# Kernel optimization log

Hardware: AMD Instinct MI355X
Metric: run time of the kernel (lower is better)

The kernel has to match this reference:

```python
import jax, jax.numpy as jnp
import numpy as np
import math

B, N, E = 4, 20000, 320000
CIN, SD, CF, TF = 4, 2, 8, 4
W, L, S, H, FFN, OUT = 256, 4, 64, 8, 1024, 4
D = W // H
EPS = 1e-6  # graph_bias_eps


def _layer_norm(x, w, b):
    mu = jnp.mean(x, -1, keepdims=True)
    var = jnp.mean((x - mu) ** 2, -1, keepdims=True)
    return (x - mu) * jax.lax.rsqrt(var + 1e-5) * w + b


def _aggregate(row, col, vals, x):
    # sparse adj (N,N) @ x per batch: y[b,i] = sum_e vals[e] * x[b, col[e]] for row[e]==i
    def one(xb):
        return jax.ops.segment_sum(vals[:, None] * xb[col], row, num_segments=N)
    return jax.vmap(one)(x)


def setup_inputs() -> dict:
    key = jax.random.key(0)
    ks = jax.random.split(key, 24)
    def n(i, shape, scale=0.02):
        return jax.random.normal(ks[i], shape, dtype=jnp.float32) * scale
    inp = {}
    inp['fields'] = jax.random.normal(ks[0], (B, N, CIN), dtype=jnp.float32)
    inp['coords'] = jax.random.uniform(ks[1], (B, N, SD), dtype=jnp.float32)
    inp['t_norm'] = jax.random.uniform(ks[2], (B,), dtype=jnp.float32)
    inp['adj_values'] = jax.random.uniform(ks[3], (E,), dtype=jnp.float32)
    # --- parameters ---
    inp['freq_matrix'] = jax.random.normal(ks[4], (SD, CF), dtype=jnp.float32)
    inp['omega'] = 1000.0 ** (-jnp.arange(TF, dtype=jnp.float32) / TF)
    inp['in_w'] = n(5, (CIN + 2 * CF + 2 * TF, W)); inp['in_b'] = jnp.zeros((W,), jnp.float32)
    inp['ln1_w'] = jnp.ones((L, W), jnp.float32); inp['ln1_b'] = jnp.zeros((L, W), jnp.float32)
    inp['ln2_w'] = jnp.ones((L, W), jnp.float32); inp['ln2_b'] = jnp.zeros((L, W), jnp.float32)
    inp['slice_w'] = n(6, (L, W, S)); inp['slice_b'] = jnp.zeros((L, S), jnp.float32)
    inp['q_w'] = n(7, (L, W, W)); inp['q_b'] = jnp.zeros((L, W), jnp.float32)
    inp['k_w'] = n(8, (L, W, W)); inp['k_b'] = jnp.zeros((L, W), jnp.float32)
    inp['v_w'] = n(9, (L, W, W)); inp['v_b'] = jnp.zeros((L, W), jnp.float32)
    inp['o_w'] = n(10, (L, W, W)); inp['o_b'] = jnp.zeros((L, W), jnp.float32)
    inp['beta_raw'] = jnp.full((L,), math.log(math.expm1(0.13)), jnp.float32)
    inp['ffn1_w'] = n(11, (L, W, FFN)); inp['ffn1_b'] = jnp.zeros((L, FFN), jnp.float32)
    inp['ffn2_w'] = n(12, (L, FFN, W)); inp['ffn2_b'] = jnp.zeros((L, W), jnp.float32)
    inp['out_w'] = n(13, (W, OUT)); inp['out_b'] = jnp.zeros((OUT,), jnp.float32)
    inp['adj_indices'] = jax.random.randint(ks[14], (2, E), 0, N, dtype=jnp.int32)
    return inp


def reference(fields, coords, t_norm, adj_values, freq_matrix, omega, in_w, in_b,
              ln1_w, ln1_b, ln2_w, ln2_b, slice_w, slice_b, q_w, q_b, k_w, k_b,
              v_w, v_b, o_w, o_b, beta_raw, ffn1_w, ffn1_b, ffn2_w, ffn2_b,
              out_w, out_b, adj_indices):
    row, col = adj_indices[0], adj_indices[1]
    # spatial + temporal encoders
    sp = 2.0 * jnp.pi * (coords @ freq_matrix)
    spat = jnp.concatenate([jnp.sin(sp), jnp.cos(sp)], -1)               # (B,N,2*CF)
    ang = (t_norm * 1000.0)[:, None] * omega[None, :]
    temb = jnp.concatenate([jnp.sin(ang), jnp.cos(ang)], -1)             # (B,2*TF)
    temb = jnp.broadcast_to(temb[:, None, :], (B, N, 2 * TF))
    h = jnp.concatenate([fields, spat, temb], -1) @ in_w + in_b          # (B,N,W)
    for l in range(L):
        # ---- GraphBiasAttention on norm1(h) ----
        hn = _layer_norm(h, ln1_w[l], ln1_b[l])
        weights = jax.nn.softmax(hn @ slice_w[l] + slice_b[l], -1)       # (B,N,S)
        wsum = jnp.maximum(weights.sum(1), EPS)                          # (B,S)
        slices = jnp.einsum('bns,bnc->bsc', weights, hn) / wsum[..., None]
        gw = _aggregate(row, col, adj_values, weights)                   # (B,N,S)
        gb = jnp.einsum('bns,bnt->bst', weights, gw)                     # (B,S,S)
        gb = 0.5 * (gb + gb.transpose(0, 2, 1))
        gb = gb / jnp.maximum(gb.sum(-1, keepdims=True), EPS)
        gb = jnp.log(jnp.maximum(gb, EPS))
        q = (slices @ q_w[l] + q_b[l]).reshape(B, S, H, D).transpose(0, 2, 1, 3)
        k = (slices @ k_w[l] + k_b[l]).reshape(B, S, H, D).transpose(0, 2, 1, 3)
        v = (slices @ v_w[l] + v_b[l]).reshape(B, S, H, D).transpose(0, 2, 1, 3)
        logits = jnp.einsum('bhsd,bhtd->bhst', q, k) / math.sqrt(D)
        logits = logits + jax.nn.softplus(beta_raw[l]) * gb[:, None]
        attn = jax.nn.softmax(logits, -1)
        so = jnp.einsum('bhst,bhtd->bhsd', attn, v).transpose(0, 2, 1, 3).reshape(B, S, W)
        so = so @ o_w[l] + o_b[l]
        h = h + jnp.einsum('bns,bsc->bnc', weights, so)
        # ---- FFN ----
        hn2 = _layer_norm(h, ln2_w[l], ln2_b[l])
        h = h + (jax.nn.gelu(hn2 @ ffn1_w[l] + ffn1_b[l], approximate=False) @ ffn2_w[l] + ffn2_b[l])
    return h @ out_w + out_b                                             # (B,N,OUT)
```

## Files before the change

### kernel.cpp

```cpp
#include <hip/hip_runtime.h>
#include <math.h>

#define BB 4
#define NN 20000
#define NE 320000
#define WW 256
#define SS 64
#define NH 8
#define HD 32
#define NF 1024
#define NL 4
#define GEPS 1e-6f

typedef __attribute__((ext_vector_type(8))) short short8v;
typedef __attribute__((ext_vector_type(4))) float f32x4;

static __device__ __forceinline__ short f2bf(float x){
  union { float f; unsigned u; } v; v.f = x;
  unsigned r = v.u + 0x7fffu + ((v.u >> 16) & 1u);
  return (short)(r >> 16);
}
static __device__ __forceinline__ float bfu_lo(unsigned u){
  union { unsigned u; float f; } v; v.u = u << 16; return v.f;
}
static __device__ __forceinline__ float bfu_hi(unsigned u){
  union { unsigned u; float f; } v; v.u = u & 0xffff0000u; return v.f;
}
static __device__ __forceinline__ float gelu_f(float x){
  return 0.5f*x*(1.0f + erff(x*0.70710678118654752f));
}

#define GLOAD16(gsrc, ldst) \
  __builtin_amdgcn_global_load_lds( \
      (const __attribute__((address_space(1))) void*)(gsrc), \
      (__attribute__((address_space(3))) void*)(ldst), 16, 0, 0)

__global__ __launch_bounds__(256) void k_embed(
    const float* __restrict__ fields, const float* __restrict__ coords,
    const float* __restrict__ t_norm, const float* __restrict__ freq,
    const float* __restrict__ omega, const float* __restrict__ in_w,
    const float* __restrict__ in_b, float* __restrict__ h)
{
  __shared__ float inv[16][28];
  __shared__ float temb[8];
  const int t = threadIdx.x;
  const size_t tok0 = (size_t)blockIdx.x * 16;
  const int b = (int)(tok0 / NN);
  if (t < 8) {
    int f = t & 3;
    float ang = t_norm[b] * 1000.0f * omega[f];
    temb[t] = (t < 4) ? sinf(ang) : cosf(ang);
  }
  if (t < 128) {
    int tok = t >> 3, f = t & 7;
    size_t n = tok0 + tok;
    float c0 = coords[n*2+0], c1 = coords[n*2+1];
    float sp = 6.283185307179586f * (c0*freq[f] + c1*freq[8+f]);
    inv[tok][4+f]  = sinf(sp);
    inv[tok][12+f] = cosf(sp);
  } else if (t < 192) {
    int idx = t - 128; int tok = idx >> 2, i = idx & 3;
    inv[tok][i] = fields[(tok0+tok)*4 + i];
  }
  __syncthreads();
  if (t < 128) {
    int tok = t >> 3, f = t & 7;
    inv[tok][20+f] = temb[f];
  }
  __syncthreads();
  float acc[16];
  float bias = in_b[t];
  #pragma unroll
  for (int i = 0; i < 16; i++) acc[i] = bias;
  #pragma unroll 4
  for (int k = 0; k < 28; k++) {
    float w = in_w[k*WW + t];
    #pragma unroll
    for (int i = 0; i < 16; i++) acc[i] += inv[i][k]*w;
  }
  #pragma unroll
  for (int i = 0; i < 16; i++) h[(tok0+i)*WW + t] = acc[i];
}

__global__ __launch_bounds__(256) void k_lnw(
    const float* __restrict__ h, const float* __restrict__ lnw,
    const float* __restrict__ lnb, const float* __restrict__ sw,
    const float* __restrict__ sb, float* __restrict__ wts,
    short* __restrict__ wtsb, float* __restrict__ mu_rstd)
{
  __shared__ float hn[16][WW];
  __shared__ float ps[16][16], pq[16][16];
  __shared__ float mus[16], rss[16];
  const int t = threadIdx.x;
  const size_t tok0 = (size_t)blockIdx.x * 16;
  const int tok = t >> 4, seg = t & 15;
  {
    const float4* hp = (const float4*)(h + (tok0+tok)*WW + seg*16);
    float sum = 0.f, sq = 0.f;
    #pragma unroll
    for (int i = 0; i < 4; i++){
      float4 v = hp[i];
      sum += v.x+v.y+v.z+v.w;
      sq  += v.x*v.x+v.y*v.y+v.z*v.z+v.w*v.w;
      *((float4*)&hn[tok][seg*16 + i*4]) = v;
    }
    ps[tok][seg] = sum; pq[tok][seg] = sq;
  }
  __syncthreads();
  if (t < 16){
    float s0=0.f, q0=0.f;
    #pragma unroll
    for (int i = 0; i < 16; i++){ s0 += ps[t][i]; q0 += pq[t][i]; }
    float mu = s0*(1.0f/WW);
    float var = q0*(1.0f/WW) - mu*mu;
    float rs = rsqrtf(var + 1e-5f);
    mus[t] = mu; rss[t] = rs;
    mu_rstd[(tok0 + t)*2]     = mu;
    mu_rstd[(tok0 + t)*2 + 1] = rs;
  }
  __syncthreads();
  {
    float mu = mus[tok], rs = rss[tok];
    #pragma unroll
    for (int i = 0; i < 16; i++){
      int c = seg*16 + i;
      hn[tok][c] = (hn[tok][c]-mu)*rs*lnw[c] + lnb[c];
    }
  }
  __syncthreads();
  const int s = t & 63, tg = t >> 6;
  float acc[4];
  float bs = sb[s];
  #pragma unroll
  for (int i = 0; i < 4; i++) acc[i] = bs;
  for (int c4 = 0; c4 < 64; c4++){
    float w0 = sw[(c4*4+0)*SS + s];
    float w1 = sw[(c4*4+1)*SS + s];
    float w2 = sw[(c4*4+2)*SS + s];
    float w3 = sw[(c4*4+3)*SS + s];
    #pragma unroll
    for (int i = 0; i < 4; i++){
      float4 hv = *((const float4*)&hn[tg*4+i][c4*4]);
      acc[i] += hv.x*w0 + hv.y*w1 + hv.z*w2 + hv.w*w3;
    }
  }
  #pragma unroll
  for (int i = 0; i < 4; i++){
    float m = acc[i];
    #pragma unroll
    for (int off = 32; off > 0; off >>= 1) m = fmaxf(m, __shfl_xor(m, off));
    float e = expf(acc[i] - m);
    float ssum = e;
    #pragma unroll
    for (int off = 32; off > 0; off >>= 1) ssum += __shfl_xor(ssum, off);
    float wv = e/ssum;
    wts[(tok0 + tg*4 + i)*SS + s] = wv;
    wtsb[(tok0 + tg*4 + i)*SS + s] = f2bf(wv);
  }
}

__global__ __launch_bounds__(256) void k_slices(
    const float* __restrict__ h, const float* __restrict__ wts,
    const float* __restrict__ mu_rstd, const float* __restrict__ lnw,
    const float* __restrict__ lnb, float* __restrict__ sacc,
    float* __restrict__ wsum)
{
  __shared__ float wstage[16][SS];
  const int t = threadIdx.x;
  const int b = blockIdx.y;
  const int n0 = blockIdx.x * 128;
  const float lw = lnw[t], lb = lnb[t];
  float acc[SS];
  #pragma unroll
  for (int s = 0; s < SS; s++) acc[s] = 0.f;
  float wsl = 0.f;
  for (int it = 0; it < 8; it++){
    int nb = n0 + it*16;
    {
      int tk = t >> 4, s4 = (t & 15)*4;
      int n = nb + tk;
      float4 v = make_float4(0.f,0.f,0.f,0.f);
      if (n < NN) v = *((const float4*)(wts + ((size_t)b*NN + n)*SS + s4));
      *((float4*)&wstage[tk][s4]) = v;
    }
    __syncthreads();
    #pragma unroll 4
    for (int tk = 0; tk < 16; tk++){
      int n = nb + tk;
      if (n < NN){
        size_t g = (size_t)b*NN + n;
        float mu = mu_rstd[g*2], rsd = mu_rstd[g*2+1];
        float hv = h[g*WW + t];
        float hnv = (hv-mu)*rsd*lw + lb;
        #pragma unroll
        for (int s4 = 0; s4 < 16; s4++){
          float4 wv = *((const float4*)&wstage[tk][s4*4]);
          acc[s4*4+0] += wv.x*hnv;
          acc[s4*4+1] += wv.y*hnv;
          acc[s4*4+2] += wv.z*hnv;
          acc[s4*4+3] += wv.w*hnv;
        }
      }
    }
    if (t < SS){
      #pragma unroll
      for (int tk = 0; tk < 16; tk++) wsl += wstage[tk][t];
    }
    __syncthreads();
  }
  #pragma unroll
  for (int s = 0; s < SS; s++)
    atomicAdd(&sacc[((size_t)b*SS + s)*WW + t], acc[s]);
  if (t < SS) atomicAdd(&wsum[b*SS + t], wsl);
}

__global__ __launch_bounds__(256) void k_slices_fin(
    const float* __restrict__ sacc, const float* __restrict__ wsum,
    float* __restrict__ slices)
{
  int i = blockIdx.x*256 + threadIdx.x;
  int sidx = i >> 8;
  float ws = fmaxf(wsum[sidx], GEPS);
  slices[i] = sacc[i] / ws;
}

#define GB_BLKS 1000
#define GB_PB   250
#define GB_EDG  (NE/GB_PB)
__global__ __launch_bounds__(256) void k_gb2(
    const short* __restrict__ wtsb, const int* __restrict__ adj,
    const float* __restrict__ vals, float* __restrict__ gb)
{
  __shared__ float gbw[SS*SS];
  const int t = threadIdx.x;
  const int bid = blockIdx.x;
  const int xcd = bid & 7;
  const int b = xcd >> 1;
  const int grp = (bid >> 3)*2 + (xcd & 1);
  const int e0 = grp * GB_EDG;
  const int w = t >> 6, l = t & 63;
  const int sg = l >> 3, tg = l & 7;
  #pragma unroll
  for (int i = 0; i < 16; i++) gbw[t + 256*i] = 0.f;
  __syncthreads();
  float acc[8][8];
  #pragma unroll
  for (int i = 0; i < 8; i++)
    #pragma unroll
    for (int u = 0; u < 8; u++) acc[i][u] = 0.f;
  const short* wb = wtsb + (size_t)b*NN*SS;
  for (int e = e0 + w; e < e0 + GB_EDG; e += 8){
    int row0 = adj[e],     col0 = adj[NE + e];
    int row1 = adj[e + 4], col1 = adj[NE + e + 4];
    float v0 = vals[e], v1 = vals[e + 4];
    uint4 ru0 = *(const uint4*)(wb + (size_t)row0*SS + sg*8);
    uint4 cu0 = *(const uint4*)(wb + (size_t)col0*SS + tg*8);
    uint4 ru1 = *(const uint4*)(wb + (size_t)row1*SS + sg*8);
    uint4 cu1 = *(const uint4*)(wb + (size_t)col1*SS + tg*8);
    float rr[8], cc[8];
    rr[0]=bfu_lo(ru0.x)*v0; rr[1]=bfu_hi(ru0.x)*v0;
    rr[2]=bfu_lo(ru0.y)*v0; rr[3]=bfu_hi(ru0.y)*v0;
    rr[4]=bfu_lo(ru0.z)*v0; rr[5]=bfu_hi(ru0.z)*v0;
    rr[6]=bfu_lo(ru0.w)*v0; rr[7]=bfu_hi(ru0.w)*v0;
    cc[0]=bfu_lo(cu0.x); cc[1]=bfu_hi(cu0.x);
    cc[2]=bfu_lo(cu0.y); cc[3]=bfu_hi(cu0.y);
    cc[4]=bfu_lo(cu0.z); cc[5]=bfu_hi(cu0.z);
    cc[6]=bfu_lo(cu0.w); cc[7]=bfu_hi(cu0.w);
    #pragma unroll
    for (int i = 0; i < 8; i++)
      #pragma unroll
      for (int u = 0; u < 8; u++) acc[i][u] += rr[i]*cc[u];
    rr[0]=bfu_lo(ru1.x)*v1; rr[1]=bfu_hi(ru1.x)*v1;
    rr[2]=bfu_lo(ru1.y)*v1; rr[3]=bfu_hi(ru1.y)*v1;
    rr[4]=bfu_lo(ru1.z)*v1; rr[5]=bfu_hi(ru1.z)*v1;
    rr[6]=bfu_lo(ru1.w)*v1; rr[7]=bfu_hi(ru1.w)*v1;
    cc[0]=bfu_lo(cu1.x); cc[1]=bfu_hi(cu1.x);
    cc[2]=bfu_lo(cu1.y); cc[3]=bfu_hi(cu1.y);
    cc[4]=bfu_lo(cu1.z); cc[5]=bfu_hi(cu1.z);
    cc[6]=bfu_lo(cu1.w); cc[7]=bfu_hi(cu1.w);
    #pragma unroll
    for (int i = 0; i < 8; i++)
      #pragma unroll
      for (int u = 0; u < 8; u++) acc[i][u] += rr[i]*cc[u];
  }
  #pragma unroll
  for (int i = 0; i < 8; i++)
    #pragma unroll
    for (int u = 0; u < 8; u++)
      atomicAdd(&gbw[(sg*8+i)*SS + tg*8 + u], acc[i][u]);
  __syncthreads();
  #pragma unroll
  for (int i = 0; i < 16; i++){
    int idx = t + 256*i;
    atomicAdd(&gb[(size_t)b*SS*SS + idx], gbw[idx]);
  }
}

__global__ __launch_bounds__(256) void k_gbfin(
    const float* __restrict__ gbin, float* __restrict__ gbout,
    const float* __restrict__ beta_raw, int layer)
{
  __shared__ float g[SS*SS];
  __shared__ float gs[SS*SS];
  __shared__ float rs[SS];
  const int t = threadIdx.x;
  const int b = blockIdx.x;
  #pragma unroll
  for (int i = 0; i < 16; i++) g[t + 256*i] = gbin[(size_t)b*SS*SS + t + 256*i];
  __syncthreads();
  #pragma unroll
  for (int i = 0; i < 16; i++){
    int idx = t + 256*i; int r = idx >> 6, c = idx & 63;
    gs[idx] = 0.5f*(g[idx] + g[c*SS + r]);
  }
  __syncthreads();
  if (t < SS){
    float sum = 0.f;
    for (int c = 0; c < SS; c++) sum += gs[t*SS + c];
    rs[t] = 1.0f / fmaxf(sum, GEPS);
  }
  __syncthreads();
  float beta = log1pf(expf(beta_raw[layer]));
  #pragma unroll
  for (int i = 0; i < 16; i++){
    int idx = t + 256*i; int r = idx >> 6;
    gbout[(size_t)b*SS*SS + idx] = beta * logf(fmaxf(gs[idx]*rs[r], GEPS));
  }
}

__global__ __launch_bounds__(256) void k_attn(
    const float* __restrict__ slices,
    const float* __restrict__ qw, const float* __restrict__ qb,
    const float* __restrict__ kw, const float* __restrict__ kb,
    const float* __restrict__ vw, const float* __restrict__ vb,
    const float* __restrict__ gbf, float* __restrict__ so)
{
  __shared__ float sl[SS][WW];
  __shared__ float qh[SS][HD], kh[SS][HD], vh[SS][HD];
  __shared__ float att[SS][SS];
  const int t = threadIdx.x;
  const int hh = blockIdx.x, b = blockIdx.y;
  {
    const float4* sp4 = (const float4*)(slices + (size_t)b*SS*WW);
    float4* sl4 = (float4*)sl;
    #pragma unroll
    for (int i = 0; i < 16; i++) sl4[t + 256*i] = sp4[t + 256*i];
  }
  __syncthreads();
  const int s = t >> 2, dq = t & 3, d0 = dq*8;
  float aq[8], ak[8], av[8];
  #pragma unroll
  for (int j = 0; j < 8; j++){
    aq[j] = qb[hh*HD + d0 + j];
    ak[j] = kb[hh*HD + d0 + j];
    av[j] = vb[hh*HD + d0 + j];
  }
  for (int c = 0; c < WW; c++){
    float sv = sl[s][c];
    const float4* q4 = (const float4*)(qw + (size_t)c*WW + hh*HD + d0);
    const float4* k4 = (const float4*)(kw + (size_t)c*WW + hh*HD + d0);
    const float4* v4 = (const float4*)(vw + (size_t)c*WW + hh*HD + d0);
    float4 qa = q4[0], qc = q4[1];
    float4 ka = k4[0], kc = k4[1];
    float4 va = v4[0], vc = v4[1];
    aq[0]+=sv*qa.x; aq[1]+=sv*qa.y; aq[2]+=sv*qa.z; aq[3]+=sv*qa.w;
    aq[4]+=sv*qc.x; aq[5]+=sv*qc.y; aq[6]+=sv*qc.z; aq[7]+=sv*qc.w;
    ak[0]+=sv*ka.x; ak[1]+=sv*ka.y; ak[2]+=sv*ka.z; ak[3]+=sv*ka.w;
    ak[4]+=sv*kc.x; ak[5]+=sv*kc.y; ak[6]+=sv*kc.z; ak[7]+=sv*kc.w;
    av[0]+=sv*va.x; av[1]+=sv*va.y; av[2]+=sv*va.z; av[3]+=sv*va.w;
    av[4]+=sv*vc.x; av[5]+=sv*vc.y; av[6]+=sv*vc.z; av[7]+=sv*vc.w;
  }
  *((float4*)&qh[s][d0])   = make_float4(aq[0],aq[1],aq[2],aq[3]);
  *((float4*)&qh[s][d0+4]) = make_float4(aq[4],aq[5],aq[6],aq[7]);
  *((float4*)&kh[s][d0])   = make_float4(ak[0],ak[1],ak[2],ak[3]);
  *((float4*)&kh[s][d0+4]) = make_float4(ak[4],ak[5],ak[6],ak[7]);
  *((float4*)&vh[s][d0])   = make_float4(av[0],av[1],av[2],av[3]);
  *((float4*)&vh[s][d0+4]) = make_float4(av[4],av[5],av[6],av[7]);
  __syncthreads();
  float qreg[HD];
  #pragma unroll
  for (int d4 = 0; d4 < 8; d4++){
    float4 qv = *((const float4*)&qh[s][d4*4]);
    qreg[d4*4+0]=qv.x; qreg[d4*4+1]=qv.y; qreg[d4*4+2]=qv.z; qreg[d4*4+3]=qv.w;
  }
  const int tc0 = dq*16;
  float lg[16];
  #pragma unroll
  for (int u = 0; u < 16; u++){
    float a = 0.f;
    #pragma unroll
    for (int d4 = 0; d4 < 8; d4++){
      float4 kv = *((const float4*)&kh[tc0+u][d4*4]);
      a += qreg[d4*4+0]*kv.x + qreg[d4*4+1]*kv.y + qreg[d4*4+2]*kv.z + qreg[d4*4+3]*kv.w;
    }
    lg[u] = a*0.17677669529663687f + gbf[((size_t)b*SS + s)*SS + tc0 + u];
  }
  float m = lg[0];
  #pragma unroll
  for (int u = 1; u < 16; u++) m = fmaxf(m, lg[u]);
  m = fmaxf(m, __shfl_xor(m, 1));
  m = fmaxf(m, __shfl_xor(m, 2));
  float ssum = 0.f;
  #pragma unroll
  for (int u = 0; u < 16; u++){ lg[u] = expf(lg[u]-m); ssum += lg[u]; }
  ssum += __shfl_xor(ssum, 1);
  ssum += __shfl_xor(ssum, 2);
  float invs = 1.0f/ssum;
  #pragma unroll
  for (int u = 0; u < 16; u++) att[s][tc0+u] = lg[u]*invs;
  __syncthreads();
  float ao[8];
  #pragma unroll
  for (int j = 0; j < 8; j++) ao[j] = 0.f;
  for (int t2 = 0; t2 < SS; t2++){
    float a = att[s][t2];
    float4 v0 = *((const float4*)&vh[t2][d0]);
    float4 v1 = *((const float4*)&vh[t2][d0+4]);
    ao[0]+=a*v0.x; ao[1]+=a*v0.y; ao[2]+=a*v0.z; ao[3]+=a*v0.w;
    ao[4]+=a*v1.x; ao[5]+=a*v1.y; ao[6]+=a*v1.z; ao[7]+=a*v1.w;
  }
  float* sop = so + ((size_t)b*SS + s)*WW + hh*HD + d0;
  *((float4*)sop)     = make_float4(ao[0],ao[1],ao[2],ao[3]);
  *((float4*)(sop+4)) = make_float4(ao[4],ao[5],ao[6],ao[7]);
}

__global__ __launch_bounds__(256) void k_oproj(
    const float* __restrict__ so, const float* __restrict__ ow,
    const float* __restrict__ ob, float* __restrict__ so_out)
{
  __shared__ float st[16][WW];
  const int t = threadIdx.x;
  const int b = blockIdx.y;
  const int s0 = blockIdx.x * 16;
  {
    const float4* sp = (const float4*)(so + ((size_t)b*SS + s0)*WW);
    float4* st4 = (float4*)st;
    #pragma unroll
    for (int i = 0; i < 4; i++) st4[t + 256*i] = sp[t + 256*i];
  }
  __syncthreads();
  float acc[16];
  float bias = ob[t];
  #pragma unroll
  for (int i = 0; i < 16; i++) acc[i] = bias;
  for (int k4 = 0; k4 < 64; k4++){
    float w0 = ow[(size_t)(k4*4+0)*WW + t];
    float w1 = ow[(size_t)(k4*4+1)*WW + t];
    float w2 = ow[(size_t)(k4*4+2)*WW + t];
    float w3 = ow[(size_t)(k4*4+3)*WW + t];
    #pragma unroll
    for (int i = 0; i < 16; i++){
      float4 sv = *((const float4*)&st[i][k4*4]);
      acc[i] += sv.x*w0 + sv.y*w1 + sv.z*w2 + sv.w*w3;
    }
  }
  #pragma unroll
  for (int i = 0; i < 16; i++)
    so_out[((size_t)b*SS + s0 + i)*WW + t] = acc[i];
}

__global__ __launch_bounds__(256) void k_hupd(
    const float* __restrict__ wts, const float* __restrict__ so_out,
    float* __restrict__ h)
{
  __shared__ float wst[64*SS];
  const int t = threadIdx.x;
  const int b = blockIdx.y;
  const int n0 = blockIdx.x * 128;
  float sc[SS];
  #pragma unroll
  for (int s = 0; s < SS; s++) sc[s] = so_out[((size_t)b*SS + s)*WW + t];
  for (int it = 0; it < 2; it++){
    int nb = n0 + it*64;
    {
      const float4* wsrc = (const float4*)(wts + ((size_t)b*NN + nb)*SS);
      #pragma unroll
      for (int i = 0; i < 4; i++){
        int jj = t + 256*i;
        int tk = jj >> 4;
        float4 v = make_float4(0.f,0.f,0.f,0.f);
        if (nb + tk < NN) v = wsrc[jj];
        *((float4*)&wst[jj*4]) = v;
      }
    }
    __syncthreads();
    for (int tk = 0; tk < 64; tk++){
      int n = nb + tk;
      if (n >= NN) break;
      float a = 0.f;
      #pragma unroll
      for (int s4 = 0; s4 < 16; s4++){
        float4 wv = *((const float4*)&wst[tk*SS + s4*4]);
        a += wv.x*sc[s4*4+0] + wv.y*sc[s4*4+1] + wv.z*sc[s4*4+2] + wv.w*sc[s4*4+3];
      }
      h[((size_t)b*NN + n)*WW + t] += a;
    }
    __syncthreads();
  }
}

__global__ __launch_bounds__(256) void k_tr1(
    const float* __restrict__ in, short* __restrict__ out)
{
  __shared__ float tile[32][33];
  const int tx = threadIdx.x & 31;
  const int ty = threadIdx.x >> 5;
  const size_t moff = (size_t)blockIdx.z * WW * NF;
  const int x = blockIdx.x*32 + tx;
  const int y0 = blockIdx.y*32;
  #pragma unroll
  for (int i = 0; i < 4; i++){
    int r = y0 + ty + i*8;
    tile[ty + i*8][tx] = in[moff + (size_t)r*NF + x];
  }
  __syncthreads();
  const int k = y0 + tx;
  #pragma unroll
  for (int i = 0; i < 4; i++){
    int j = blockIdx.x*32 + ty + i*8;
    int off = j*WW + ((((k>>3) ^ (j&7)))<<3) + (k&7);
    out[moff + off] = f2bf(tile[tx][ty + i*8]);
  }
}

__global__ __launch_bounds__(256) void k_tr2(
    const float* __restrict__ in, short* __restrict__ out)
{
  __shared__ float tile[32][33];
  const int tx = threadIdx.x & 31;
  const int ty = threadIdx.x >> 5;
  const size_t moff = (size_t)blockIdx.z * NF * WW;
  const int x = blockIdx.x*32 + tx;
  const int y0 = blockIdx.y*32;
  #pragma unroll
  for (int i = 0; i < 4; i++){
    int r = y0 + ty + i*8;
    tile[ty + i*8][tx] = in[moff + (size_t)r*WW + x];
  }
  __syncthreads();
  const int ch = y0 >> 5;
  const int jl = tx;
  #pragma unroll
  for (int i = 0; i < 4; i++){
    int c = blockIdx.x*32 + ty + i*8;
    int off = ch*8192 + c*32 + ((((jl>>3) ^ (c&3)))<<3) + (jl&7);
    out[moff + off] = f2bf(tile[tx][ty + i*8]);
  }
}

#define FTM 64
#define CH 32
__global__ __launch_bounds__(256, 4) void k_ffn7(
    float* __restrict__ h,
    const float* __restrict__ lnw, const float* __restrict__ lnb,
    const short* __restrict__ w1t, const float* __restrict__ b1,
    const short* __restrict__ w2t, const float* __restrict__ b2)
{
  __align__(16) __shared__ short w1s[CH*256];
  __align__(16) __shared__ short w2s[256*CH];
  __align__(16) __shared__ short gbuf[4][16*40];
  const int t = threadIdx.x;
  const int w = t >> 6, l = t & 63;
  const int lm = l & 15, g = l >> 4;
  const size_t tok0 = (size_t)blockIdx.x * FTM;
  const size_t tokA = tok0 + (size_t)w*16 + lm;
  short8v hn[8];
  {
    const float* hp = h + tokA*WW + g*8;
    float4 hv[16];
    float sum = 0.f, sq = 0.f;
    #pragma unroll
    for (int u = 0; u < 16; u++){
      float4 v = *(const float4*)(hp + (u>>1)*32 + (u&1)*4);
      hv[u] = v;
      sum += v.x+v.y+v.z+v.w;
      sq  += v.x*v.x+v.y*v.y+v.z*v.z+v.w*v.w;
    }
    sum += __shfl_xor(sum, 16); sum += __shfl_xor(sum, 32);
    sq  += __shfl_xor(sq, 16);  sq  += __shfl_xor(sq, 32);
    float mu = sum*(1.0f/WW);
    float var = sq*(1.0f/WW) - mu*mu;
    float rs = rsqrtf(var + 1e-5f);
    #pragma unroll
    for (int f = 0; f < 8; f++){
      float4 w0 = *(const float4*)(lnw + f*32 + g*8);
      float4 w1 = *(const float4*)(lnw + f*32 + g*8 + 4);
      float4 b0 = *(const float4*)(lnb + f*32 + g*8);
      float4 b1v = *(const float4*)(lnb + f*32 + g*8 + 4);
      float4 a = hv[f*2], bqv = hv[f*2+1];
      short8v fr;
      fr[0] = f2bf((a.x  -mu)*rs*w0.x + b0.x);
      fr[1] = f2bf((a.y  -mu)*rs*w0.y + b0.y);
      fr[2] = f2bf((a.z  -mu)*rs*w0.z + b0.z);
      fr[3] = f2bf((a.w  -mu)*rs*w0.w + b0.w);
      fr[4] = f2bf((bqv.x-mu)*rs*w1.x + b1v.x);
      fr[5] = f2bf((bqv.y-mu)*rs*w1.y + b1v.y);
      fr[6] = f2bf((bqv.z-mu)*rs*w1.z + b1v.z);
      fr[7] = f2bf((bqv.w-mu)*rs*w1.w + b1v.w);
      hn[f] = fr;
    }
  }
  f32x4 acc2[16];
  #pragma unroll
  for (int ct = 0; ct < 16; ct++)
    acc2[ct] = (f32x4){0.f,0.f,0.f,0.f};

  for (int ch = 0; ch < NF/CH; ch++){
    const int j0 = ch*CH;
    const short* w1c = w1t + (size_t)j0*256;
    const short* w2c = w2t + (size_t)ch*8192;
    #pragma unroll
    for (int it = 0; it < 4; it++){
      int p = w*4 + it;
      GLOAD16(w1c + p*512 + l*8, w1s + p*512);
      GLOAD16(w2c + p*512 + l*8, w2s + p*512);
    }
    __syncthreads();
    #pragma unroll
    for (int jt = 0; jt < 2; jt++){
      f32x4 d0 = (f32x4){0.f,0.f,0.f,0.f};
      const int rl = jt*16 + lm;
      #pragma unroll
      for (int ks = 0; ks < 8; ks++){
        short8v af = *(const short8v*)(w1s + rl*256 + ((((ks<<2)|g) ^ (rl&7))<<3));
        d0 = __builtin_amdgcn_mfma_f32_16x16x32_bf16(af, hn[ks], d0, 0, 0, 0);
      }
      float4 bb = *(const float4*)(b1 + j0 + jt*16 + g*4);
      float x0 = gelu_f(d0[0] + bb.x), x1 = gelu_f(d0[1] + bb.y);
      float x2 = gelu_f(d0[2] + bb.z), x3 = gelu_f(d0[3] + bb.w);
      unsigned u0 = (unsigned)(unsigned short)f2bf(x0) | ((unsigned)(unsigned short)f2bf(x1) << 16);
      unsigned u1 = (unsigned)(unsigned short)f2bf(x2) | ((unsigned)(unsigned short)f2bf(x3) << 16);
      *(uint2*)(&gbuf[w][lm*40 + jt*16 + g*4]) = make_uint2(u0, u1);
    }
    short8v gA0 = *(const short8v*)(&gbuf[w][lm*40 + g*8]);
    #pragma unroll
    for (int ct = 0; ct < 16; ct++){
      const int row = ct*16 + lm;
      short8v a0 = *(const short8v*)(w2s + row*32 + (((g ^ (row&3)))<<3));
      acc2[ct] = __builtin_amdgcn_mfma_f32_16x16x32_bf16(a0, gA0, acc2[ct], 0, 0, 0);
    }
    __syncthreads();
  }
  float* tb = (float*)&gbuf[w][0];
  const int tok_l = l >> 2, cq = (l & 3)*4;
  {
    const size_t trow = tok0 + (size_t)w*16;
    #pragma unroll
    for (int ct = 0; ct < 16; ct++){
      float4 sv;
      sv.x = acc2[ct][0]; sv.y = acc2[ct][1];
      sv.z = acc2[ct][2]; sv.w = acc2[ct][3];
      *(float4*)(&tb[lm*20 + g*4]) = sv;
      float4 tv = *(const float4*)(&tb[tok_l*20 + cq]);
      float4 bb = *(const float4*)(b2 + ct*16 + cq);
      float* hp = h + (trow + tok_l)*WW + ct*16 + cq;
      float4 ho = *(const float4*)hp;
      ho.x += tv.x + bb.x; ho.y += tv.y + bb.y;
      ho.z += tv.z + bb.z; ho.w += tv.w + bb.w;
      *(float4*)hp = ho;
    }
  }
}

__global__ __launch_bounds__(256) void k_out(
    const float* __restrict__ h, const float* __restrict__ ow,
    const float* __restrict__ ob, float* __restrict__ out)
{
  size_t n = (size_t)blockIdx.x*256 + threadIdx.x;
  if (n >= (size_t)BB*NN) return;
  float a0=ob[0], a1=ob[1], a2=ob[2], a3=ob[3];
  const float4* hp = (const float4*)(h + n*WW);
  const float4* ow4 = (const float4*)ow;
  for (int c4 = 0; c4 < 64; c4++){
    float4 hv = hp[c4];
    float4 w0 = ow4[c4*4+0], w1 = ow4[c4*4+1], w2 = ow4[c4*4+2], w3 = ow4[c4*4+3];
    a0 += hv.x*w0.x + hv.y*w1.x + hv.z*w2.x + hv.w*w3.x;
    a1 += hv.x*w0.y + hv.y*w1.y + hv.z*w2.y + hv.w*w3.y;
    a2 += hv.x*w0.z + hv.y*w1.z + hv.z*w2.z + hv.w*w3.z;
    a3 += hv.x*w0.w + hv.y*w1.w + hv.z*w2.w + hv.w*w3.w;
  }
  *((float4*)(out + n*4)) = make_float4(a0,a1,a2,a3);
}

extern "C" void kernel_launch(void* const* d_in, const int* in_sizes, int n_in,
                              void* d_out, int out_size, void* d_ws, size_t ws_size,
                              hipStream_t stream) {
  const float* fields    = (const float*)d_in[0];
  const float* coords    = (const float*)d_in[1];
  const float* t_norm    = (const float*)d_in[2];
  const float* adj_vals  = (const float*)d_in[3];
  const float* freq      = (const float*)d_in[4];
  const float* omega     = (const float*)d_in[5];
  const float* in_w      = (const float*)d_in[6];
  const float* in_b      = (const float*)d_in[7];
  const float* ln1_w     = (const float*)d_in[8];
  const float* ln1_b     = (const float*)d_in[9];
  const float* ln2_w     = (const float*)d_in[10];
  const float* ln2_b     = (const float*)d_in[11];
  const float* slice_w   = (const float*)d_in[12];
  const float* slice_b   = (const float*)d_in[13];
  const float* q_w       = (const float*)d_in[14];
  const float* q_b       = (const float*)d_in[15];
  const float* k_w       = (const float*)d_in[16];
  const float* k_b       = (const float*)d_in[17];
  const float* v_w       = (const float*)d_in[18];
  const float* v_b       = (const float*)d_in[19];
  const float* o_w       = (const float*)d_in[20];
  const float* o_b       = (const float*)d_in[21];
  const float* beta_raw  = (const float*)d_in[22];
  const float* ffn1_w    = (const float*)d_in[23];
  const float* ffn1_b    = (const float*)d_in[24];
  const float* ffn2_w    = (const float*)d_in[25];
  const float* ffn2_b    = (const float*)d_in[26];
  const float* out_w     = (const float*)d_in[27];
  const float* out_b     = (const float*)d_in[28];
  const int*   adj       = (const int*)d_in[29];
  float* out = (float*)d_out;

  float* ws = (float*)d_ws;
  size_t off = 0;
  float* h        = ws + off; off += (size_t)BB*NN*WW;
  float* wts      = ws + off; off += (size_t)BB*NN*SS;
  float* mu_rstd  = ws + off; off += (size_t)BB*NN*2;
  float* sacc     = ws + off; off += (size_t)BB*SS*WW;
  float* wsumb    = ws + off; off += (size_t)BB*SS;
  float* gb       = ws + off; off += (size_t)BB*SS*SS;
  float* gbf      = ws + off; off += (size_t)BB*SS*SS;
  float* slices   = ws + off; off += (size_t)BB*SS*WW;
  float* so       = ws + off; off += (size_t)BB*SS*WW;
  float* so_out   = ws + off; off += (size_t)BB*SS*WW;
  short* w1tb     = (short*)(ws + off); off += (size_t)NL*WW*NF/2;
  short* w2tb     = (short*)(ws + off); off += (size_t)NL*WW*NF/2;
  short* wtsb     = (short*)(ws + off); off += (size_t)BB*NN*SS/2;

  hipLaunchKernelGGL(k_tr1, dim3(NF/32, WW/32, NL), dim3(256), 0, stream,
      ffn1_w, w1tb);
  hipLaunchKernelGGL(k_tr2, dim3(WW/32, NF/32, NL), dim3(256), 0, stream,
      ffn2_w, w2tb);

  hipLaunchKernelGGL(k_embed, dim3(BB*NN/16), dim3(256), 0, stream,
      fields, coords, t_norm, freq, omega, in_w, in_b, h);

  for (int l = 0; l < NL; l++){
    hipMemsetAsync(sacc, 0,
        (size_t)(BB*SS*WW + BB*SS + BB*SS*SS)*sizeof(float), stream);
    hipLaunchKernelGGL(k_lnw, dim3(BB*NN/16), dim3(256), 0, stream,
        h, ln1_w + l*WW, ln1_b + l*WW,
        slice_w + (size_t)l*WW*SS, slice_b + l*SS, wts, wtsb, mu_rstd);
    hipLaunchKernelGGL(k_slices, dim3(157, BB), dim3(256), 0, stream,
        h, wts, mu_rstd, ln1_w + l*WW, ln1_b + l*WW, sacc, wsumb);
    hipLaunchKernelGGL(k_slices_fin, dim3(BB*SS*WW/256), dim3(256), 0, stream,
        sacc, wsumb, slices);
    hipLaunchKernelGGL(k_gb2, dim3(GB_BLKS), dim3(256), 0, stream,
        wtsb, adj, adj_vals, gb);
    hipLaunchKernelGGL(k_gbfin, dim3(BB), dim3(256), 0, stream,
        gb, gbf, beta_raw, l);
    hipLaunchKernelGGL(k_attn, dim3(NH, BB), dim3(256), 0, stream,
        slices,
        q_w + (size_t)l*WW*WW, q_b + l*WW,
        k_w + (size_t)l*WW*WW, k_b + l*WW,
        v_w + (size_t)l*WW*WW, v_b + l*WW,
        gbf, so);
    hipLaunchKernelGGL(k_oproj, dim3(4, BB), dim3(256), 0, stream,
        so, o_w + (size_t)l*WW*WW, o_b + l*WW, so_out);
    hipLaunchKernelGGL(k_hupd, dim3(157, BB), dim3(256), 0, stream,
        wts, so_out, h);
    hipLaunchKernelGGL(k_ffn7, dim3(BB*NN/FTM), dim3(256), 0, stream,
        h, ln2_w + l*WW, ln2_b + l*WW,
        w1tb + (size_t)l*WW*NF, ffn1_b + l*NF,
        w2tb + (size_t)l*WW*NF, ffn2_b + l*WW);
  }

  hipLaunchKernelGGL(k_out, dim3((BB*NN + 255)/256), dim3(256), 0, stream,
      h, out_w, out_b, out);
}
```

Measured before the change: 3.684 ms.

## Fuse slice-attention residual update into FFN kernel

Removes the separate k_hupd kernel and performs the weights@so_out residual update at the start of the FFN kernel. so_out is staged in shared memory in two halves, and the updated h feeds the layernorm statistics directly. This saves one full read-modify-write pass over h and one launch per layer. In exchange the grid becomes 2D per batch with a validity guard, and each token does its S=64 update with FP32 FMAs, which adds register pressure under the 4-blocks-per-CU launch bound.

```diff
diff --git a/kernel.cpp b/kernel.cpp
--- a/kernel.cpp
+++ b/kernel.cpp
@@ -459,46 +459,6 @@
     so_out[((size_t)b*SS + s0 + i)*WW + t] = acc[i];
 }
 
-__global__ __launch_bounds__(256) void k_hupd(
-    const float* __restrict__ wts, const float* __restrict__ so_out,
-    float* __restrict__ h)
-{
-  __shared__ float wst[64*SS];
-  const int t = threadIdx.x;
-  const int b = blockIdx.y;
-  const int n0 = blockIdx.x * 128;
-  float sc[SS];
-  #pragma unroll
-  for (int s = 0; s < SS; s++) sc[s] = so_out[((size_t)b*SS + s)*WW + t];
-  for (int it = 0; it < 2; it++){
-    int nb = n0 + it*64;
-    {
-      const float4* wsrc = (const float4*)(wts + ((size_t)b*NN + nb)*SS);
-      #pragma unroll
-      for (int i = 0; i < 4; i++){
-        int jj = t + 256*i;
-        int tk = jj >> 4;
-        float4 v = make_float4(0.f,0.f,0.f,0.f);
-        if (nb + tk < NN) v = wsrc[jj];
-        *((float4*)&wst[jj*4]) = v;
-      }
-    }
-    __syncthreads();
-    for (int tk = 0; tk < 64; tk++){
-      int n = nb + tk;
-      if (n >= NN) break;
-      float a = 0.f;
-      #pragma unroll
-      for (int s4 = 0; s4 < 16; s4++){
-        float4 wv = *((const float4*)&wst[tk*SS + s4*4]);
-        a += wv.x*sc[s4*4+0] + wv.y*sc[s4*4+1] + wv.z*sc[s4*4+2] + wv.w*sc[s4*4+3];
-      }
-      h[((size_t)b*NN + n)*WW + t] += a;
-    }
-    __syncthreads();
-  }
-}
-
 __global__ __launch_bounds__(256) void k_tr1(
     const float* __restrict__ in, short* __restrict__ out)
 {
@@ -550,60 +510,103 @@
 
 #define FTM 64
 #define CH 32
-__global__ __launch_bounds__(256, 4) void k_ffn7(
-    float* __restrict__ h,
+__global__ __launch_bounds__(256, 4) void k_ffn8(
+    float* __restrict__ h, const float* __restrict__ wts,
+    const float* __restrict__ so_out,
     const float* __restrict__ lnw, const float* __restrict__ lnb,
     const short* __restrict__ w1t, const float* __restrict__ b1,
     const short* __restrict__ w2t, const float* __restrict__ b2)
 {
-  __align__(16) __shared__ short w1s[CH*256];
-  __align__(16) __shared__ short w2s[256*CH];
+  __shared__ __align__(16) char wbig[32768];
   __align__(16) __shared__ short gbuf[4][16*40];
+  short* w1s = (short*)wbig;
+  short* w2s = (short*)(wbig + 16384);
+  float* sob = (float*)wbig;
   const int t = threadIdx.x;
   const int w = t >> 6, l = t & 63;
   const int lm = l & 15, g = l >> 4;
-  const size_t tok0 = (size_t)blockIdx.x * FTM;
-  const size_t tokA = tok0 + (size_t)w*16 + lm;
+  const int b = blockIdx.y;
+  const int ltok0 = blockIdx.x * FTM;
+  const bool valid = (ltok0 + w*16) < NN;
+  const int lA = valid ? (ltok0 + w*16 + lm) : lm;
+  const size_t tokA = (size_t)b*NN + lA;
+  float* hrow = h + tokA*WW;
+  const float* wrow = wts + tokA*SS;
+
+  float sum = 0.f, sq = 0.f;
+  #pragma unroll
+  for (int half = 0; half < 2; half++){
+    __syncthreads();
+    #pragma unroll
+    for (int it = 0; it < 8; it++){
+      int idx = it*256 + t;
+      int s = idx >> 5, c4 = (idx & 31) << 2;
+      GLOAD16(so_out + ((size_t)b*SS + s)*WW + half*128 + c4,
+              ((float*)sob) + (size_t)idx*4);
+    }
+    __syncthreads();
+    float4 hv[8], upd[8];
+    #pragma unroll
+    for (int u = 0; u < 8; u++){
+      hv[u] = *(const float4*)(hrow + (half*4 + (u>>1))*32 + g*8 + (u&1)*4);
+      upd[u] = make_float4(0.f,0.f,0.f,0.f);
+    }
+    #pragma unroll 2
+    for (int s4 = 0; s4 < 16; s4++){
+      float4 wv4 = *(const float4*)(wrow + s4*4);
+      #pragma unroll
+      for (int k = 0; k < 4; k++){
+        float wv = (k==0)?wv4.x:(k==1)?wv4.y:(k==2)?wv4.z:wv4.w;
+        const float* sor = sob + (s4*4+k)*128 + g*8;
+        #pragma unroll
+        for (int u = 0; u < 8; u++){
+          float4 so4 = *(const float4*)(sor + (u>>1)*32 + (u&1)*4);
+          upd[u].x += wv*so4.x; upd[u].y += wv*so4.y;
+          upd[u].z += wv*so4.z; upd[u].w += wv*so4.w;
+        }
+      }
+    }
+    #pragma unroll
+    for (int u = 0; u < 8; u++){
+      float4 nv;
+      nv.x = hv[u].x + upd[u].x; nv.y = hv[u].y + upd[u].y;
+      nv.z = hv[u].z + upd[u].z; nv.w = hv[u].w + upd[u].w;
+      sum += nv.x+nv.y+nv.z+nv.w;
+      sq  += nv.x*nv.x+nv.y*nv.y+nv.z*nv.z+nv.w*nv.w;
+      if (valid)
+        *(float4*)(hrow + (half*4 + (u>>1))*32 + g*8 + (u&1)*4) = nv;
+    }
+  }
+  sum += __shfl_xor(sum, 16); sum += __shfl_xor(sum, 32);
+  sq  += __shfl_xor(sq, 16);  sq  += __shfl_xor(sq, 32);
+  float mu = sum*(1.0f/WW);
+  float var = sq*(1.0f/WW) - mu*mu;
+  float rs = rsqrtf(var + 1e-5f);
   short8v hn[8];
-  {
-    const float* hp = h + tokA*WW + g*8;
-    float4 hv[16];
-    float sum = 0.f, sq = 0.f;
-    #pragma unroll
-    for (int u = 0; u < 16; u++){
-      float4 v = *(const float4*)(hp + (u>>1)*32 + (u&1)*4);
-      hv[u] = v;
-      sum += v.x+v.y+v.z+v.w;
-      sq  += v.x*v.x+v.y*v.y+v.z*v.z+v.w*v.w;
-    }
-    sum += __shfl_xor(sum, 16); sum += __shfl_xor(sum, 32);
-    sq  += __shfl_xor(sq, 16);  sq  += __shfl_xor(sq, 32);
-    float mu = sum*(1.0f/WW);
-    float var = sq*(1.0f/WW) - mu*mu;
-    float rs = rsqrtf(var + 1e-5f);
-    #pragma unroll
-    for (int f = 0; f < 8; f++){
-      float4 w0 = *(const float4*)(lnw + f*32 + g*8);
-      float4 w1 = *(const float4*)(lnw + f*32 + g*8 + 4);
-      float4 b0 = *(const float4*)(lnb + f*32 + g*8);
-      float4 b1v = *(const float4*)(lnb + f*32 + g*8 + 4);
-      float4 a = hv[f*2], bqv = hv[f*2+1];
-      short8v fr;
-      fr[0] = f2bf((a.x  -mu)*rs*w0.x + b0.x);
-      fr[1] = f2bf((a.y  -mu)*rs*w0.y + b0.y);
-      fr[2] = f2bf((a.z  -mu)*rs*w0.z + b0.z);
-      fr[3] = f2bf((a.w  -mu)*rs*w0.w + b0.w);
-      fr[4] = f2bf((bqv.x-mu)*rs*w1.x + b1v.x);
-      fr[5] = f2bf((bqv.y-mu)*rs*w1.y + b1v.y);
-      fr[6] = f2bf((bqv.z-mu)*rs*w1.z + b1v.z);
-      fr[7] = f2bf((bqv.w-mu)*rs*w1.w + b1v.w);
-      hn[f] = fr;
-    }
+  #pragma unroll
+  for (int f = 0; f < 8; f++){
+    float4 a  = *(const float4*)(hrow + f*32 + g*8);
+    float4 bq = *(const float4*)(hrow + f*32 + g*8 + 4);
+    float4 w0 = *(const float4*)(lnw + f*32 + g*8);
+    float4 w1 = *(const float4*)(lnw + f*32 + g*8 + 4);
+    float4 b0 = *(const float4*)(lnb + f*32 + g*8);
+    float4 b1v = *(const float4*)(lnb + f*32 + g*8 + 4);
+    short8v fr;
+    fr[0] = f2bf((a.x -mu)*rs*w0.x + b0.x);
+    fr[1] = f2bf((a.y -mu)*rs*w0.y + b0.y);
+    fr[2] = f2bf((a.z -mu)*rs*w0.z + b0.z);
+    fr[3] = f2bf((a.w -mu)*rs*w0.w + b0.w);
+    fr[4] = f2bf((bq.x-mu)*rs*w1.x + b1v.x);
+    fr[5] = f2bf((bq.y-mu)*rs*w1.y + b1v.y);
+    fr[6] = f2bf((bq.z-mu)*rs*w1.z + b1v.z);
+    fr[7] = f2bf((bq.w-mu)*rs*w1.w + b1v.w);
+    hn[f] = fr;
   }
   f32x4 acc2[16];
   #pragma unroll
   for (int ct = 0; ct < 16; ct++)
     acc2[ct] = (f32x4){0.f,0.f,0.f,0.f};
+  __syncthreads();
 
   for (int ch = 0; ch < NF/CH; ch++){
     const int j0 = ch*CH;
@@ -641,10 +644,10 @@
     }
     __syncthreads();
   }
-  float* tb = (float*)&gbuf[w][0];
-  const int tok_l = l >> 2, cq = (l & 3)*4;
-  {
-    const size_t trow = tok0 + (size_t)w*16;
+  if (valid){
+    float* tb = (float*)&gbuf[w][0];
+    const int tok_l = l >> 2, cq = (l & 3)*4;
+    const size_t trow = (size_t)b*NN + ltok0 + w*16;
     #pragma unroll
     for (int ct = 0; ct < 16; ct++){
       float4 sv;
@@ -763,10 +766,8 @@
         gbf, so);
     hipLaunchKernelGGL(k_oproj, dim3(4, BB), dim3(256), 0, stream,
         so, o_w + (size_t)l*WW*WW, o_b + l*WW, so_out);
-    hipLaunchKernelGGL(k_hupd, dim3(157, BB), dim3(256), 0, stream,
-        wts, so_out, h);
-    hipLaunchKernelGGL(k_ffn7, dim3(BB*NN/FTM), dim3(256), 0, stream,
-        h, ln2_w + l*WW, ln2_b + l*WW,
+    hipLaunchKernelGGL(k_ffn8, dim3((NN + FTM - 1)/FTM, BB), dim3(256), 0, stream,
+        h, wts, so_out, ln2_w + l*WW, ln2_b + l*WW,
         w1tb + (size_t)l*WW*NF, ffn1_b + l*NF,
         w2tb + (size_t)l*WW*NF, ffn2_b + l*WW);
   }
```

Measured after the change: 3.129 ms. -15.0%, faster.
